# Performance work log

Measured on AMD Instinct MI355X. Metric: run time of the kernel, lower is better.

The kernel has to match this reference:

```python
import jax, jax.numpy as jnp
import numpy as np

DIM = 1024
HEADS = 16
DIM_HEAD = 64
INNER = HEADS * DIM_HEAD  # 1024
B, N = 2, 2048


def setup_inputs() -> dict:
    key = jax.random.key(0)
    ks = jax.random.split(key, 6)
    x = jax.random.normal(ks[0], (B, N, DIM), dtype=jnp.float32)
    rel_pos_bias = jax.random.normal(ks[1], (1, HEADS, N, N), dtype=jnp.float32)
    g = jnp.ones((DIM,), dtype=jnp.float32)
    # Linear weights stored torch-style as [out_features, in_features].
    # Note: original zero-inits Wo; we use small random values so outputs/grads are non-trivial.
    Wq = jax.random.normal(ks[2], (INNER, DIM), dtype=jnp.float32) * (DIM ** -0.5)
    Wkv = jax.random.normal(ks[3], (2 * INNER, DIM), dtype=jnp.float32) * (DIM ** -0.5)
    Wo = jax.random.normal(ks[4], (DIM, INNER), dtype=jnp.float32) * (INNER ** -0.5)
    return {"x": x, "rel_pos_bias": rel_pos_bias, "g": g, "Wq": Wq, "Wkv": Wkv, "Wo": Wo}


def reference(x, rel_pos_bias, g, Wq, Wkv, Wo):
    eps = 1e-5  # x is float32
    # Faithful to source: normalize over dim=1 (sequence axis), biased variance.
    mean = jnp.mean(x, axis=1, keepdims=True)          # [b, 1, d]
    var = jnp.var(x, axis=1, keepdims=True)            # [b, 1, d]
    xn = (x - mean) * jax.lax.rsqrt(jnp.maximum(var, eps)) * g

    q = xn @ Wq.T                                      # [b, n, inner]
    kv = xn @ Wkv.T                                    # [b, n, 2*inner]
    k, v = jnp.split(kv, 2, axis=-1)

    def to_heads(t):  # b n (h d) -> b h n d
        b, n, _ = t.shape
        return t.reshape(b, n, HEADS, DIM_HEAD).transpose(0, 2, 1, 3)

    q, k, v = to_heads(q), to_heads(k), to_heads(v)
    q = q * (DIM_HEAD ** -0.5)

    sim = jnp.einsum('bhid,bhjd->bhij', q, k) + rel_pos_bias  # [b, h, n, n]
    attn = jax.nn.softmax(sim, axis=-1)
    out = jnp.einsum('bhij,bhjd->bhid', attn, v)              # [b, h, n, d]
    out = out.transpose(0, 2, 1, 3).reshape(x.shape[0], x.shape[1], INNER)
    return out @ Wo.T                                         # [b, n, dim]
```

## Files before the change

kernel.cpp:

```cpp
#include <hip/hip_runtime.h>
#include <hip/hip_bf16.h>

typedef __bf16 bf16;
typedef __attribute__((ext_vector_type(8))) __bf16 bf16x8;
typedef __attribute__((ext_vector_type(4))) __bf16 bf16x4;
typedef __attribute__((ext_vector_type(4))) float f32x4;
typedef __attribute__((ext_vector_type(16))) float f32x16;
typedef __attribute__((ext_vector_type(4))) unsigned int u32x4;

#define DIMD  1024
#define SEQ   2048
#define BATCH 2
#define HEADS 16
#define INNER 1024
#define QKVN  3072
#define ROWS  (BATCH*SEQ)
#define LOG2E 1.44269504f

__global__ void ln_partial(const float* __restrict__ x,
                           float* __restrict__ psum, float* __restrict__ psq) {
    const int nc = blockIdx.x;
    const int b  = blockIdx.y;
    const int t  = threadIdx.x;
    const float* xp = x + ((size_t)b*SEQ + (size_t)nc*32)*DIMD;
    float s0=0,s1=0,s2=0,s3=0,q0=0,q1=0,q2=0,q3=0;
    for (int r=0; r<32; ++r) {
        const float* row = xp + (size_t)r*DIMD;
        float v0=row[t], v1=row[t+256], v2=row[t+512], v3=row[t+768];
        s0+=v0; q0+=v0*v0; s1+=v1; q1+=v1*v1;
        s2+=v2; q2+=v2*v2; s3+=v3; q3+=v3*v3;
    }
    float* ps = psum + ((size_t)b*64 + nc)*DIMD;
    float* pq = psq  + ((size_t)b*64 + nc)*DIMD;
    ps[t]=s0; ps[t+256]=s1; ps[t+512]=s2; ps[t+768]=s3;
    pq[t]=q0; pq[t+256]=q1; pq[t+512]=q2; pq[t+768]=q3;
}

__global__ void ln_finalize(const float* __restrict__ psum, const float* __restrict__ psq,
                            const float* __restrict__ g,
                            float* __restrict__ scale, float* __restrict__ shift) {
    const int d = blockIdx.x*256 + threadIdx.x;
    const int b = blockIdx.y;
    float s=0.f, q=0.f;
    for (int nc=0; nc<64; ++nc) {
        s += psum[((size_t)b*64+nc)*DIMD + d];
        q += psq [((size_t)b*64+nc)*DIMD + d];
    }
    const float inv_n = 1.f/(float)SEQ;
    float mean = s*inv_n;
    float var  = q*inv_n - mean*mean;
    var = fmaxf(var, 1e-5f);
    scale[b*DIMD+d] = g[d]*rsqrtf(var);
    shift[b*DIMD+d] = mean;
}

__global__ void ln_apply(const float* __restrict__ x,
                         const float* __restrict__ scale, const float* __restrict__ shift,
                         bf16* __restrict__ xn) {
    size_t idx = ((size_t)blockIdx.x*256 + threadIdx.x)*4;
    int b = (int)(idx >> 21);
    int d = (int)(idx & (DIMD-1));
    f32x4 v  = *reinterpret_cast<const f32x4*>(x + idx);
    f32x4 sc = *reinterpret_cast<const f32x4*>(scale + (size_t)b*DIMD + d);
    f32x4 sh = *reinterpret_cast<const f32x4*>(shift + (size_t)b*DIMD + d);
    bf16x4 o;
    o.x = (bf16)((v.x - sh.x)*sc.x);
    o.y = (bf16)((v.y - sh.y)*sc.y);
    o.z = (bf16)((v.z - sh.z)*sc.z);
    o.w = (bf16)((v.w - sh.w)*sc.w);
    *reinterpret_cast<bf16x4*>(xn + idx) = o;
}

__global__ void castk(const float* __restrict__ s, bf16* __restrict__ d, int n, float scl) {
    int i = (blockIdx.x*256 + threadIdx.x)*4;
    if (i >= n) return;
    f32x4 v = *reinterpret_cast<const f32x4*>(s + i);
    bf16x4 o; o.x=(bf16)(v.x*scl); o.y=(bf16)(v.y*scl); o.z=(bf16)(v.z*scl); o.w=(bf16)(v.w*scl);
    *reinterpret_cast<bf16x4*>(d + i) = o;
}

__device__ __forceinline__ void gload16(const void* g, void* l) {
    __builtin_amdgcn_global_load_lds(
        (const __attribute__((address_space(1))) unsigned int*)g,
        (__attribute__((address_space(3))) unsigned int*)l,
        16, 0, 0);
}

__device__ inline void store_out(float* p, float v) { *p = v; }
__device__ inline void store_out(bf16*  p, float v) { *p = (bf16)v; }

template <typename OT>
__global__ __launch_bounds__(256, 2)
void gemm_bt(const bf16* __restrict__ A, const bf16* __restrict__ B,
             OT* __restrict__ C, int M, int N, int K) {
    __shared__ bf16 As[128*64];
    __shared__ bf16 Bs[128*64];
    const int t = threadIdx.x;
    const int wave = t >> 6, lane = t & 63;
    const int wr = wave >> 1, wc = wave & 1;
    const int m0 = blockIdx.y*128, n0 = blockIdx.x*128;
    const int lr = lane & 15, lg = lane >> 4;
    const int srow = wave*32 + (lane>>3);
    const int scol = (lane&7)*8;

    f32x4 acc[4][4];
    #pragma unroll
    for (int i=0;i<4;++i)
        #pragma unroll
        for (int j=0;j<4;++j) acc[i][j] = (f32x4){0.f,0.f,0.f,0.f};

    for (int k0=0; k0<K; k0+=64) {
        #pragma unroll
        for (int i=0;i<4;++i) {
            gload16(A + (size_t)(m0+srow+8*i)*K + k0 + scol, As + (srow+8*i)*64 + scol);
            gload16(B + (size_t)(n0+srow+8*i)*K + k0 + scol, Bs + (srow+8*i)*64 + scol);
        }
        __syncthreads();
        #pragma unroll
        for (int kk=0; kk<2; ++kk) {
            bf16x8 a[4], b[4];
            #pragma unroll
            for (int mi=0;mi<4;++mi)
                a[mi] = *reinterpret_cast<const bf16x8*>(As + (wr*64+mi*16+lr)*64 + kk*32+lg*8);
            #pragma unroll
            for (int ni=0;ni<4;++ni)
                b[ni] = *reinterpret_cast<const bf16x8*>(Bs + (wc*64+ni*16+lr)*64 + kk*32+lg*8);
            #pragma unroll
            for (int mi=0;mi<4;++mi)
                #pragma unroll
                for (int ni=0;ni<4;++ni)
                    acc[mi][ni] = __builtin_amdgcn_mfma_f32_16x16x32_bf16(a[mi], b[ni], acc[mi][ni], 0, 0, 0);
        }
        __syncthreads();
    }
    #pragma unroll
    for (int mi=0;mi<4;++mi)
        #pragma unroll
        for (int ni=0;ni<4;++ni)
            #pragma unroll
            for (int r=0;r<4;++r) {
                int row = m0 + wr*64 + mi*16 + lg*4 + r;
                int col = n0 + wc*64 + ni*16 + lr;
                store_out(&C[(size_t)row*N + col], acc[mi][ni][r]);
            }
}

__global__ __launch_bounds__(256)
void transpose_v(const bf16* __restrict__ qkv, bf16* __restrict__ vT) {
    __shared__ bf16 tile[64][72];
    const int nt = blockIdx.x, h = blockIdx.y, b = blockIdx.z;
    const int t = threadIdx.x;
    const bf16* src = qkv + ((size_t)(b*SEQ + nt*64))*QKVN + 2*INNER + h*64;
    #pragma unroll
    for (int i=0;i<2;++i) {
        int c = t + 256*i, row = c>>3, col = (c&7)*8;
        *reinterpret_cast<bf16x8*>(&tile[row][col]) =
            *reinterpret_cast<const bf16x8*>(src + (size_t)row*QKVN + col);
    }
    __syncthreads();
    bf16* dst = vT + ((size_t)(b*HEADS + h))*64*SEQ + nt*64;
    #pragma unroll
    for (int i=0;i<2;++i) {
        int c = t + 256*i, d = c>>3, n0 = (c&7)*8;
        bf16x8 v;
        #pragma unroll
        for (int j=0;j<8;++j) v[j] = tile[n0+j][d];
        *reinterpret_cast<bf16x8*>(dst + (size_t)d*SEQ + n0) = v;
    }
}


__device__ __forceinline__ unsigned pk2(float a, float b) {
    union { bf16 h[2]; unsigned u; } x;
    x.h[0] = (bf16)a; x.h[1] = (bf16)b;
    return x.u;
}

#define ATTN_BARRIER()                                         \
    __builtin_amdgcn_sched_barrier(0);                         \
    asm volatile("s_waitcnt lgkmcnt(0)" ::: "memory");         \
    __builtin_amdgcn_s_barrier();                              \
    __builtin_amdgcn_sched_barrier(0)

#define ATTN_ITER(CUR, T)                                                          \
  {                                                                                \
                                      \
    if ((T)+1 < 32) {                                                              \
      *reinterpret_cast<bf16x8*>(&Ks[(CUR)^1][st_off])        = kr0;               \
      *reinterpret_cast<bf16x8*>(&Ks[(CUR)^1][st_off+2048])   = kr1;               \
      *reinterpret_cast<bf16x8*>(&VTs[(CUR)^1][st_off])       = vr0;               \
      *reinterpret_cast<bf16x8*>(&VTs[(CUR)^1][st_off+2048])  = vr1;               \
    }                                                                              \
                   \
    if ((T)+2 < 32) {                                                              \
      kr0 = *reinterpret_cast<const bf16x8*>(kbase + (size_t)(((T)+2)*64+srow)*QKVN + scol);   \
      kr1 = *reinterpret_cast<const bf16x8*>(kbase + (size_t)(((T)+2)*64+srow+32)*QKVN + scol);\
      vr0 = *reinterpret_cast<const bf16x8*>(vtb + (size_t)srow*SEQ + ((T)+2)*64 + scol);      \
      vr1 = *reinterpret_cast<const bf16x8*>(vtb + (size_t)(srow+32)*SEQ + ((T)+2)*64 + scol); \
    }                                                                              \
                                                 \
    if ((T)+1 < 32) {                                                              \
      _Pragma("unroll")                                                            \
      for (int B2=0;B2<2;++B2)                                                     \
        _Pragma("unroll")                                                          \
        for (int rr=0;rr<4;++rr)                                                   \
          breg[(CUR)^1][B2][rr] = *reinterpret_cast<const f32x4*>(                 \
              brow + ((T)+1)*64 + 32*B2 + 8*rr);                                   \
    }                                                                              \
                                    \
    f32x16 p0 = (f32x16)(0.0f), p1 = (f32x16)(0.0f);                               \
    __builtin_amdgcn_s_setprio(1);                                                 \
    _Pragma("unroll")                                                              \
    for (int s=0;s<4;++s) {                                                        \
      bf16x8 kf0 = *reinterpret_cast<const bf16x8*>(&Ks[CUR][koff[0][s]]);         \
      p0 = __builtin_amdgcn_mfma_f32_32x32x16_bf16(kf0, qf[s], p0, 0,0,0);         \
      bf16x8 kf1 = *reinterpret_cast<const bf16x8*>(&Ks[CUR][koff[1][s]]);         \
      p1 = __builtin_amdgcn_mfma_f32_32x32x16_bf16(kf1, qf[s], p1, 0,0,0);         \
    }                                                                              \
    __builtin_amdgcn_s_setprio(0);                                                 \
            \
    float v0[16], v1[16];                                                          \
    _Pragma("unroll")                                                              \
    for (int r=0;r<16;++r) {                                                       \
      v0[r] = __builtin_fmaf(breg[CUR][0][r>>2][r&3], LOG2E, p0[r]);               \
      v1[r] = __builtin_fmaf(breg[CUR][1][r>>2][r&3], LOG2E, p1[r]);               \
    }                                                                              \
    float mx[8];                                                                   \
    _Pragma("unroll")                                                              \
    for (int i=0;i<8;++i)                                                          \
      mx[i] = fmaxf(fmaxf(v0[i], v0[i+8]), fmaxf(v1[i], v1[i+8]));                 \
    _Pragma("unroll")                                                              \
    for (int i=0;i<4;++i) mx[i] = fmaxf(mx[i], mx[i+4]);                           \
    float vmax = fmaxf(fmaxf(mx[0],mx[2]), fmaxf(mx[1],mx[3]));                    \
    vmax = fmaxf(vmax, __shfl_xor(vmax, 32));                                      \
    if (!__all(vmax <= m + 11.5f)) {                                               \
      float mnew = fmaxf(m, vmax);                                                 \
      float sc = __builtin_amdgcn_exp2f(m - mnew);                                 \
      m = mnew; l *= sc;                                                           \
      _Pragma("unroll")                                                            \
      for (int r=0;r<16;++r) {                                                     \
        float scr = __shfl(sc, (r&3)+8*(r>>2)+4*hi);                               \
        accO0[r] *= scr; accO1[r] *= scr;                                          \
      }                                                                            \
    }                                                                              \
    float e0[16], e1[16];                                                          \
    _Pragma("unroll")                                                              \
    for (int r=0;r<16;++r) {                                                       \
      e0[r] = __builtin_amdgcn_exp2f(v0[r] - m);                                   \
      e1[r] = __builtin_amdgcn_exp2f(v1[r] - m);                                   \
    }                                                                              \
    float sm[8];                                                                   \
    _Pragma("unroll")                                                              \
    for (int i=0;i<8;++i) sm[i] = (e0[i]+e0[i+8]) + (e1[i]+e1[i+8]);               \
    _Pragma("unroll")                                                              \
    for (int i=0;i<4;++i) sm[i] += sm[i+4];                                        \
    float rsum = (sm[0]+sm[2]) + (sm[1]+sm[3]);                                    \
    rsum += __shfl_xor(rsum, 32);                                                  \
    l += rsum;                                                                     \
           \
    unsigned W0[4][2], W1[4][2];                                                   \
    _Pragma("unroll")                                                              \
    for (int rr=0;rr<4;++rr) {                                                     \
      W0[rr][0] = pk2(e0[4*rr+0], e0[4*rr+1]);                                     \
      W0[rr][1] = pk2(e0[4*rr+2], e0[4*rr+3]);                                     \
      W1[rr][0] = pk2(e1[4*rr+0], e1[4*rr+1]);                                     \
      W1[rr][1] = pk2(e1[4*rr+2], e1[4*rr+3]);                                     \
    }                                                                              \
                               \
    bf16x8 pa[4];                                                                  \
    _Pragma("unroll")                                                              \
    for (int s4=0;s4<4;++s4) {                                                     \
      unsigned u[4];                                                               \
      _Pragma("unroll")                                                            \
      for (int hh=0;hh<2;++hh) {                                                   \
        unsigned a0 = (s4>>1) ? W1[2*(s4&1)  ][hh] : W0[2*(s4&1)  ][hh];           \
        unsigned a1 = (s4>>1) ? W1[2*(s4&1)+1][hh] : W0[2*(s4&1)+1][hh];           \
        unsigned X = hi ? a0 : a1;                                                 \
        unsigned R = (unsigned)__shfl_xor((int)X, 32);                             \
        u[hh]   = hi ? R  : a0;                                                    \
        u[2+hh] = hi ? a1 : R;                                                     \
      }                                                                            \
      u32x4 uv = {u[0], u[1], u[2], u[3]};                                         \
      pa[s4] = __builtin_bit_cast(bf16x8, uv);                                     \
    }                                                                              \
                                                                        \
    __builtin_amdgcn_s_setprio(1);                                                 \
    _Pragma("unroll")                                                              \
    for (int s4=0;s4<4;++s4) {                                                     \
      bf16x8 vfa = *reinterpret_cast<const bf16x8*>(&VTs[CUR][voff[0][s4]]);       \
      accO0 = __builtin_amdgcn_mfma_f32_32x32x16_bf16(pa[s4], vfa, accO0, 0,0,0);  \
      bf16x8 vfb = *reinterpret_cast<const bf16x8*>(&VTs[CUR][voff[1][s4]]);       \
      accO1 = __builtin_amdgcn_mfma_f32_32x32x16_bf16(pa[s4], vfb, accO1, 0,0,0);  \
    }                                                                              \
    __builtin_amdgcn_s_setprio(0);                                                 \
    ATTN_BARRIER();                                                                \
  }

__global__ __launch_bounds__(256, 2)
void attn_kernel(const bf16* __restrict__ qkv, const bf16* __restrict__ vTg,
                 const float* __restrict__ bias, bf16* __restrict__ oh) {
    __shared__ bf16 Ks[2][64*64];
    __shared__ bf16 VTs[2][64*64];

    const int b = blockIdx.x, qt = blockIdx.y, h = blockIdx.z;
    const int t = threadIdx.x;
    const int w = t >> 6, lane = t & 63;
    const int ql = lane & 31, hi = lane >> 5;
    const int q0 = qt*128;

    int koff[2][4], voff[2][4];
    #pragma unroll
    for (int B2=0;B2<2;++B2)
        #pragma unroll
        for (int s=0;s<4;++s) {
            koff[B2][s] = (32*B2+ql)*64 + (((2*s+hi) ^ (ql&7))*8);
            voff[B2][s] = (32*B2+ql)*64 + (((2*s+hi) ^ (ql&7))*8);
        }

    const int srow = t>>3;
    const int scol = (t&7)*8;
    const int st_off = srow*64 + (((t&7) ^ (srow&7))*8);

    const bf16* qrow = qkv + ((size_t)(b*SEQ + q0 + w*32 + ql))*QKVN + h*64 + hi*8;
    bf16x8 qf[4];
    #pragma unroll
    for (int s=0;s<4;++s)
        qf[s] = *reinterpret_cast<const bf16x8*>(qrow + 16*s);

    const bf16* kbase = qkv + (size_t)b*SEQ*QKVN + INNER + h*64;
    const bf16* vtb   = vTg + (size_t)(b*HEADS + h)*64*SEQ;
    const float* brow = bias + ((size_t)h*SEQ + (size_t)(q0 + w*32 + ql))*SEQ + 4*hi;

    bf16x8 kr0, kr1, vr0, vr1;
    f32x4 breg[2][2][4];

    *reinterpret_cast<bf16x8*>(&Ks[0][st_off]) =
        *reinterpret_cast<const bf16x8*>(kbase + (size_t)srow*QKVN + scol);
    *reinterpret_cast<bf16x8*>(&Ks[0][st_off+2048]) =
        *reinterpret_cast<const bf16x8*>(kbase + (size_t)(srow+32)*QKVN + scol);
    *reinterpret_cast<bf16x8*>(&VTs[0][st_off]) =
        *reinterpret_cast<const bf16x8*>(vtb + (size_t)srow*SEQ + scol);
    *reinterpret_cast<bf16x8*>(&VTs[0][st_off+2048]) =
        *reinterpret_cast<const bf16x8*>(vtb + (size_t)(srow+32)*SEQ + scol);
    kr0 = *reinterpret_cast<const bf16x8*>(kbase + (size_t)(64+srow)*QKVN + scol);
    kr1 = *reinterpret_cast<const bf16x8*>(kbase + (size_t)(64+srow+32)*QKVN + scol);
    vr0 = *reinterpret_cast<const bf16x8*>(vtb + (size_t)srow*SEQ + 64 + scol);
    vr1 = *reinterpret_cast<const bf16x8*>(vtb + (size_t)(srow+32)*SEQ + 64 + scol);
    #pragma unroll
    for (int B2=0;B2<2;++B2)
        #pragma unroll
        for (int rr=0;rr<4;++rr)
            breg[0][B2][rr] = *reinterpret_cast<const f32x4*>(brow + 32*B2 + 8*rr);
    ATTN_BARRIER();

    float m = -__builtin_inff();
    float l = 0.f;
    f32x16 accO0 = (f32x16)(0.0f), accO1 = (f32x16)(0.0f);

    for (int t2 = 0; t2 < 32; t2 += 2) {
        ATTN_ITER(0, t2);
        ATTN_ITER(1, t2+1);
    }

    float linv = 1.f/l;
    bf16* ob = oh + ((size_t)(b*SEQ + q0 + w*32))*INNER + h*64 + ql;
    #pragma unroll
    for (int r=0;r<16;++r) {
        int qoff = (r&3) + 8*(r>>2) + 4*hi;
        float li = __shfl(linv, qoff);
        ob[(size_t)qoff*INNER]      = (bf16)(accO0[r]*li);
        ob[(size_t)qoff*INNER + 32] = (bf16)(accO1[r]*li);
    }
}

extern "C" void kernel_launch(void* const* d_in, const int* in_sizes, int n_in,
                              void* d_out, int out_size, void* d_ws, size_t ws_size,
                              hipStream_t stream) {
    const float* x    = (const float*)d_in[0];
    const float* bias = (const float*)d_in[1];
    const float* g    = (const float*)d_in[2];
    const float* Wq   = (const float*)d_in[3];
    const float* Wkv  = (const float*)d_in[4];
    const float* Wo   = (const float*)d_in[5];
    float* out = (float*)d_out;

    char* ws = (char*)d_ws;
    bf16*  xn    = (bf16*)(ws);
    bf16*  vT    = (bf16*)(ws);
    bf16*  wqkv  = (bf16*)(ws + 8388608);
    bf16*  wo    = (bf16*)(ws + 14680064);
    bf16*  qkv   = (bf16*)(ws + 16777216);
    bf16*  oh    = (bf16*)(ws + 41943040);
    float* psum  = (float*)(ws + 50331648);
    float* psq   = (float*)(ws + 50855936);
    float* scale = (float*)(ws + 51380224);
    float* shift = (float*)(ws + 51388416);

    ln_partial <<<dim3(64,2), 256, 0, stream>>>(x, psum, psq);
    ln_finalize<<<dim3(4,2),  256, 0, stream>>>(psum, psq, g, scale, shift);
    ln_apply   <<<dim3(4096), 256, 0, stream>>>(x, scale, shift, xn);

    castk<<<dim3(1024), 256, 0, stream>>>(Wq,  wqkv,           1048576, 0.125f*LOG2E);
    castk<<<dim3(2048), 256, 0, stream>>>(Wkv, wqkv + 1048576, 2097152, 1.0f);
    castk<<<dim3(1024), 256, 0, stream>>>(Wo,  wo,             1048576, 1.0f);

    gemm_bt<bf16><<<dim3(24,32), 256, 0, stream>>>(xn, wqkv, qkv, ROWS, QKVN, DIMD);

    transpose_v<<<dim3(32,16,2), 256, 0, stream>>>(qkv, vT);

    attn_kernel<<<dim3(2,16,16), 256, 0, stream>>>(qkv, vT, bias, oh);

    gemm_bt<float><<<dim3(8,32), 256, 0, stream>>>(oh, wo, out, ROWS, INNER, INNER);
}
```

Measured before the change: 208.9 us.

## Stage relative-position bias through per-wave LDS with coalesced row loads

Result: no change. 208.6 us, median of 2 (-0.2%).

```diff
diff --git a/kernel.cpp b/kernel.cpp
--- a/kernel.cpp
+++ b/kernel.cpp
@@ -191,6 +191,11 @@
       *reinterpret_cast<bf16x8*>(&VTs[(CUR)^1][st_off])       = vr0;               \
       *reinterpret_cast<bf16x8*>(&VTs[(CUR)^1][st_off+2048])  = vr1;               \
     }                                                                              \
+                             \
+    _Pragma("unroll")                                                              \
+    for (int i=0;i<8;++i)                                                          \
+      *reinterpret_cast<f32x4*>(&myB[bw_off[i]]) = breg[i];                        \
+    asm volatile("" ::: "memory");                                                 \
                    \
     if ((T)+2 < 32) {                                                              \
       kr0 = *reinterpret_cast<const bf16x8*>(kbase + (size_t)(((T)+2)*64+srow)*QKVN + scol);   \
@@ -198,14 +203,11 @@
       vr0 = *reinterpret_cast<const bf16x8*>(vtb + (size_t)srow*SEQ + ((T)+2)*64 + scol);      \
       vr1 = *reinterpret_cast<const bf16x8*>(vtb + (size_t)(srow+32)*SEQ + ((T)+2)*64 + scol); \
     }                                                                              \
-                                                 \
+                  \
     if ((T)+1 < 32) {                                                              \
       _Pragma("unroll")                                                            \
-      for (int B2=0;B2<2;++B2)                                                     \
-        _Pragma("unroll")                                                          \
-        for (int rr=0;rr<4;++rr)                                                   \
-          breg[(CUR)^1][B2][rr] = *reinterpret_cast<const f32x4*>(                 \
-              brow + ((T)+1)*64 + 32*B2 + 8*rr);                                   \
+      for (int i=0;i<8;++i)                                                        \
+        breg[i] = *reinterpret_cast<const f32x4*>(bstage + (size_t)(4*i)*SEQ + ((T)+1)*64);    \
     }                                                                              \
                                     \
     f32x16 p0 = (f32x16)(0.0f), p1 = (f32x16)(0.0f);                               \
@@ -218,12 +220,19 @@
       p1 = __builtin_amdgcn_mfma_f32_32x32x16_bf16(kf1, qf[s], p1, 0,0,0);         \
     }                                                                              \
     __builtin_amdgcn_s_setprio(0);                                                 \
+                              \
+    f32x4 bb0[4], bb1[4];                                                          \
+    _Pragma("unroll")                                                              \
+    for (int rr=0;rr<4;++rr) {                                                     \
+      bb0[rr] = *reinterpret_cast<const f32x4*>(&myB[br_off[0][rr]]);              \
+      bb1[rr] = *reinterpret_cast<const f32x4*>(&myB[br_off[1][rr]]);              \
+    }                                                                              \
             \
     float v0[16], v1[16];                                                          \
     _Pragma("unroll")                                                              \
     for (int r=0;r<16;++r) {                                                       \
-      v0[r] = __builtin_fmaf(breg[CUR][0][r>>2][r&3], LOG2E, p0[r]);               \
-      v1[r] = __builtin_fmaf(breg[CUR][1][r>>2][r&3], LOG2E, p1[r]);               \
+      v0[r] = __builtin_fmaf(bb0[r>>2][r&3], LOG2E, p0[r]);                        \
+      v1[r] = __builtin_fmaf(bb1[r>>2][r&3], LOG2E, p1[r]);                        \
     }                                                                              \
     float mx[8];                                                                   \
     _Pragma("unroll")                                                              \
@@ -301,6 +310,7 @@
                  const float* __restrict__ bias, bf16* __restrict__ oh) {
     __shared__ bf16 Ks[2][64*64];
     __shared__ bf16 VTs[2][64*64];
+    __shared__ float biasLds[4*32*64];
 
     const int b = blockIdx.x, qt = blockIdx.y, h = blockIdx.z;
     const int t = threadIdx.x;
@@ -317,6 +327,23 @@
             voff[B2][s] = (32*B2+ql)*64 + (((2*s+hi) ^ (ql&7))*8);
         }
 
+    float* myB = biasLds + w*2048;
+    int bw_off[8];
+    #pragma unroll
+    for (int i=0;i<8;++i) {
+        int rw = 4*i + (lane>>4);
+        int gp = (lane&15) ^ (rw&15);
+        bw_off[i] = rw*64 + gp*4;
+    }
+    int br_off[2][4];
+    #pragma unroll
+    for (int B2=0;B2<2;++B2)
+        #pragma unroll
+        for (int rr=0;rr<4;++rr) {
+            int gp = (8*B2+2*rr+hi) ^ (ql&15);
+            br_off[B2][rr] = ql*64 + gp*4;
+        }
+
     const int srow = t>>3;
     const int scol = (t&7)*8;
     const int st_off = srow*64 + (((t&7) ^ (srow&7))*8);
@@ -329,10 +356,10 @@
 
     const bf16* kbase = qkv + (size_t)b*SEQ*QKVN + INNER + h*64;
     const bf16* vtb   = vTg + (size_t)(b*HEADS + h)*64*SEQ;
-    const float* brow = bias + ((size_t)h*SEQ + (size_t)(q0 + w*32 + ql))*SEQ + 4*hi;
+    const float* bstage = bias + ((size_t)h*SEQ + (size_t)(q0 + w*32 + (lane>>4)))*SEQ + 4*(lane&15);
 
     bf16x8 kr0, kr1, vr0, vr1;
-    f32x4 breg[2][2][4];
+    f32x4 breg[8];
 
     *reinterpret_cast<bf16x8*>(&Ks[0][st_off]) =
         *reinterpret_cast<const bf16x8*>(kbase + (size_t)srow*QKVN + scol);
@@ -347,10 +374,8 @@
     vr0 = *reinterpret_cast<const bf16x8*>(vtb + (size_t)srow*SEQ + 64 + scol);
     vr1 = *reinterpret_cast<const bf16x8*>(vtb + (size_t)(srow+32)*SEQ + 64 + scol);
     #pragma unroll
-    for (int B2=0;B2<2;++B2)
-        #pragma unroll
-        for (int rr=0;rr<4;++rr)
-            breg[0][B2][rr] = *reinterpret_cast<const f32x4*>(brow + 32*B2 + 8*rr);
+    for (int i=0;i<8;++i)
+        breg[i] = *reinterpret_cast<const f32x4*>(bstage + (size_t)(4*i)*SEQ);
     ATTN_BARRIER();
 
     float m = -__builtin_inff();
```

## Merge both batches into one 512-thread attention block sharing bias tile loads

Applied to the files above, without the earlier changes.

Result: no change. 211.6 us (+1.3%).

```diff
diff --git a/kernel.cpp b/kernel.cpp
--- a/kernel.cpp
+++ b/kernel.cpp
@@ -184,21 +184,21 @@
 
 #define ATTN_ITER(CUR, T)                                                          \
   {                                                                                \
-                                      \
+                       \
     if ((T)+1 < 32) {                                                              \
-      *reinterpret_cast<bf16x8*>(&Ks[(CUR)^1][st_off])        = kr0;               \
-      *reinterpret_cast<bf16x8*>(&Ks[(CUR)^1][st_off+2048])   = kr1;               \
-      *reinterpret_cast<bf16x8*>(&VTs[(CUR)^1][st_off])       = vr0;               \
-      *reinterpret_cast<bf16x8*>(&VTs[(CUR)^1][st_off+2048])  = vr1;               \
+      *reinterpret_cast<bf16x8*>(&Ks[0][(CUR)^1][st_off])  = krA;                  \
+      *reinterpret_cast<bf16x8*>(&Ks[1][(CUR)^1][st_off])  = krB;                  \
+      *reinterpret_cast<bf16x8*>(&VTs[0][(CUR)^1][st_off]) = vrA;                  \
+      *reinterpret_cast<bf16x8*>(&VTs[1][(CUR)^1][st_off]) = vrB;                  \
     }                                                                              \
                    \
     if ((T)+2 < 32) {                                                              \
-      kr0 = *reinterpret_cast<const bf16x8*>(kbase + (size_t)(((T)+2)*64+srow)*QKVN + scol);   \
-      kr1 = *reinterpret_cast<const bf16x8*>(kbase + (size_t)(((T)+2)*64+srow+32)*QKVN + scol);\
-      vr0 = *reinterpret_cast<const bf16x8*>(vtb + (size_t)srow*SEQ + ((T)+2)*64 + scol);      \
-      vr1 = *reinterpret_cast<const bf16x8*>(vtb + (size_t)(srow+32)*SEQ + ((T)+2)*64 + scol); \
-    }                                                                              \
-                                                 \
+      krA = *reinterpret_cast<const bf16x8*>(kbase0 + (size_t)(((T)+2)*64+srow)*QKVN + scol);  \
+      krB = *reinterpret_cast<const bf16x8*>(kbase1 + (size_t)(((T)+2)*64+srow)*QKVN + scol);  \
+      vrA = *reinterpret_cast<const bf16x8*>(vtb0 + (size_t)srow*SEQ + ((T)+2)*64 + scol);     \
+      vrB = *reinterpret_cast<const bf16x8*>(vtb1 + (size_t)srow*SEQ + ((T)+2)*64 + scol);     \
+    }                                                                              \
+          \
     if ((T)+1 < 32) {                                                              \
       _Pragma("unroll")                                                            \
       for (int B2=0;B2<2;++B2)                                                     \
@@ -212,9 +212,9 @@
     __builtin_amdgcn_s_setprio(1);                                                 \
     _Pragma("unroll")                                                              \
     for (int s=0;s<4;++s) {                                                        \
-      bf16x8 kf0 = *reinterpret_cast<const bf16x8*>(&Ks[CUR][koff[0][s]]);         \
+      bf16x8 kf0 = *reinterpret_cast<const bf16x8*>(&myK[(CUR)*4096 + koff[0][s]]); \
       p0 = __builtin_amdgcn_mfma_f32_32x32x16_bf16(kf0, qf[s], p0, 0,0,0);         \
-      bf16x8 kf1 = *reinterpret_cast<const bf16x8*>(&Ks[CUR][koff[1][s]]);         \
+      bf16x8 kf1 = *reinterpret_cast<const bf16x8*>(&myK[(CUR)*4096 + koff[1][s]]); \
       p1 = __builtin_amdgcn_mfma_f32_32x32x16_bf16(kf1, qf[s], p1, 0,0,0);         \
     }                                                                              \
     __builtin_amdgcn_s_setprio(0);                                                 \
@@ -287,24 +287,26 @@
     __builtin_amdgcn_s_setprio(1);                                                 \
     _Pragma("unroll")                                                              \
     for (int s4=0;s4<4;++s4) {                                                     \
-      bf16x8 vfa = *reinterpret_cast<const bf16x8*>(&VTs[CUR][voff[0][s4]]);       \
+      bf16x8 vfa = *reinterpret_cast<const bf16x8*>(&myV[(CUR)*4096 + voff[0][s4]]); \
       accO0 = __builtin_amdgcn_mfma_f32_32x32x16_bf16(pa[s4], vfa, accO0, 0,0,0);  \
-      bf16x8 vfb = *reinterpret_cast<const bf16x8*>(&VTs[CUR][voff[1][s4]]);       \
+      bf16x8 vfb = *reinterpret_cast<const bf16x8*>(&myV[(CUR)*4096 + voff[1][s4]]); \
       accO1 = __builtin_amdgcn_mfma_f32_32x32x16_bf16(pa[s4], vfb, accO1, 0,0,0);  \
     }                                                                              \
     __builtin_amdgcn_s_setprio(0);                                                 \
     ATTN_BARRIER();                                                                \
   }
 
-__global__ __launch_bounds__(256, 2)
+__global__ __launch_bounds__(512, 2)
 void attn_kernel(const bf16* __restrict__ qkv, const bf16* __restrict__ vTg,
                  const float* __restrict__ bias, bf16* __restrict__ oh) {
-    __shared__ bf16 Ks[2][64*64];
-    __shared__ bf16 VTs[2][64*64];
-
-    const int b = blockIdx.x, qt = blockIdx.y, h = blockIdx.z;
+    __shared__ bf16 Ks[2][2][64*64];
+    __shared__ bf16 VTs[2][2][64*64];
+
+    const int qt = blockIdx.x, h = blockIdx.y;
     const int t = threadIdx.x;
     const int w = t >> 6, lane = t & 63;
+    const int wb = w >> 2;
+    const int wq = w & 3;
     const int ql = lane & 31, hi = lane >> 5;
     const int q0 = qt*128;
 
@@ -316,36 +318,40 @@
             koff[B2][s] = (32*B2+ql)*64 + (((2*s+hi) ^ (ql&7))*8);
             voff[B2][s] = (32*B2+ql)*64 + (((2*s+hi) ^ (ql&7))*8);
         }
+    bf16* myK = (bf16*)Ks[wb];
+    bf16* myV = (bf16*)VTs[wb];
 
     const int srow = t>>3;
     const int scol = (t&7)*8;
     const int st_off = srow*64 + (((t&7) ^ (srow&7))*8);
 
-    const bf16* qrow = qkv + ((size_t)(b*SEQ + q0 + w*32 + ql))*QKVN + h*64 + hi*8;
+    const bf16* qrow = qkv + ((size_t)(wb*SEQ + q0 + wq*32 + ql))*QKVN + h*64 + hi*8;
     bf16x8 qf[4];
     #pragma unroll
     for (int s=0;s<4;++s)
         qf[s] = *reinterpret_cast<const bf16x8*>(qrow + 16*s);
 
-    const bf16* kbase = qkv + (size_t)b*SEQ*QKVN + INNER + h*64;
-    const bf16* vtb   = vTg + (size_t)(b*HEADS + h)*64*SEQ;
-    const float* brow = bias + ((size_t)h*SEQ + (size_t)(q0 + w*32 + ql))*SEQ + 4*hi;
-
-    bf16x8 kr0, kr1, vr0, vr1;
+    const bf16* kbase0 = qkv + INNER + h*64;
+    const bf16* kbase1 = qkv + (size_t)SEQ*QKVN + INNER + h*64;
+    const bf16* vtb0   = vTg + (size_t)h*64*SEQ;
+    const bf16* vtb1   = vTg + (size_t)(HEADS + h)*64*SEQ;
+    const float* brow = bias + ((size_t)h*SEQ + (size_t)(q0 + wq*32 + ql))*SEQ + 4*hi;
+
+    bf16x8 krA, krB, vrA, vrB;
     f32x4 breg[2][2][4];
 
-    *reinterpret_cast<bf16x8*>(&Ks[0][st_off]) =
-        *reinterpret_cast<const bf16x8*>(kbase + (size_t)srow*QKVN + scol);
-    *reinterpret_cast<bf16x8*>(&Ks[0][st_off+2048]) =
-        *reinterpret_cast<const bf16x8*>(kbase + (size_t)(srow+32)*QKVN + scol);
-    *reinterpret_cast<bf16x8*>(&VTs[0][st_off]) =
-        *reinterpret_cast<const bf16x8*>(vtb + (size_t)srow*SEQ + scol);
-    *reinterpret_cast<bf16x8*>(&VTs[0][st_off+2048]) =
-        *reinterpret_cast<const bf16x8*>(vtb + (size_t)(srow+32)*SEQ + scol);
-    kr0 = *reinterpret_cast<const bf16x8*>(kbase + (size_t)(64+srow)*QKVN + scol);
-    kr1 = *reinterpret_cast<const bf16x8*>(kbase + (size_t)(64+srow+32)*QKVN + scol);
-    vr0 = *reinterpret_cast<const bf16x8*>(vtb + (size_t)srow*SEQ + 64 + scol);
-    vr1 = *reinterpret_cast<const bf16x8*>(vtb + (size_t)(srow+32)*SEQ + 64 + scol);
+    *reinterpret_cast<bf16x8*>(&Ks[0][0][st_off]) =
+        *reinterpret_cast<const bf16x8*>(kbase0 + (size_t)srow*QKVN + scol);
+    *reinterpret_cast<bf16x8*>(&Ks[1][0][st_off]) =
+        *reinterpret_cast<const bf16x8*>(kbase1 + (size_t)srow*QKVN + scol);
+    *reinterpret_cast<bf16x8*>(&VTs[0][0][st_off]) =
+        *reinterpret_cast<const bf16x8*>(vtb0 + (size_t)srow*SEQ + scol);
+    *reinterpret_cast<bf16x8*>(&VTs[1][0][st_off]) =
+        *reinterpret_cast<const bf16x8*>(vtb1 + (size_t)srow*SEQ + scol);
+    krA = *reinterpret_cast<const bf16x8*>(kbase0 + (size_t)(64+srow)*QKVN + scol);
+    krB = *reinterpret_cast<const bf16x8*>(kbase1 + (size_t)(64+srow)*QKVN + scol);
+    vrA = *reinterpret_cast<const bf16x8*>(vtb0 + (size_t)srow*SEQ + 64 + scol);
+    vrB = *reinterpret_cast<const bf16x8*>(vtb1 + (size_t)srow*SEQ + 64 + scol);
     #pragma unroll
     for (int B2=0;B2<2;++B2)
         #pragma unroll
@@ -363,7 +369,7 @@
     }
 
     float linv = 1.f/l;
-    bf16* ob = oh + ((size_t)(b*SEQ + q0 + w*32))*INNER + h*64 + ql;
+    bf16* ob = oh + ((size_t)(wb*SEQ + q0 + wq*32))*INNER + h*64 + ql;
     #pragma unroll
     for (int r=0;r<16;++r) {
         int qoff = (r&3) + 8*(r>>2) + 4*hi;
@@ -408,7 +414,7 @@
 
     transpose_v<<<dim3(32,16,2), 256, 0, stream>>>(qkv, vT);
 
-    attn_kernel<<<dim3(2,16,16), 256, 0, stream>>>(qkv, vT, bias, oh);
+    attn_kernel<<<dim3(16,16), 512, 0, stream>>>(qkv, vT, bias, oh);
 
     gemm_bt<float><<<dim3(8,32), 256, 0, stream>>>(oh, wo, out, ROWS, INNER, INNER);
 }
```
